# Performance work log

Measured on AMD Instinct MI355X. Metric: run time of the kernel, lower is better.

## Reference

```python
import jax, jax.numpy as jnp
import numpy as np

M, K, N = 4096, 7168, 18432  # tokens, in_features, out_features


def setup_inputs() -> dict:
    key = jax.random.key(0)
    kx, kw, ks = jax.random.split(key, 3)
    x = jax.random.normal(kx, (M, K), dtype=jnp.float32)
    # int8 quantized weight, layout [in_features, out_features] as in the torch module
    weight = jax.random.randint(kw, (K, N), -128, 128, dtype=jnp.int8)
    # per-output-channel dequant scale (bf16 in the original; fp32 here for a stable baseline)
    scale = jax.random.uniform(ks, (N,), dtype=jnp.float32) * 0.02 + 1e-3
    return {"x": x, "weight": weight, "scale": scale}


def reference(x, weight, scale):
    # Fused dequant + GEMM: y = x @ (int8_weight * scale_per_out_channel)
    w = weight.astype(x.dtype) * scale.astype(x.dtype)[None, :]  # [K, N]
    return x @ w  # [M, N]
```

## Files before the change

### kernel.cpp

```cpp
#include <hip/hip_runtime.h>
#include <hip/hip_bf16.h>
#include <cstdint>
#include <cstddef>

#define M_ 4096
#define K_ 7168
#define N_ 18432
#define NT 56

typedef __attribute__((ext_vector_type(4))) int i32x4;
typedef __attribute__((ext_vector_type(16))) int i32x16;

#define AS1 __attribute__((address_space(1)))
#define AS3 __attribute__((address_space(3)))

__device__ __forceinline__ void gld_lds16(void* lds, const void* g) {
  __builtin_amdgcn_global_load_lds((const AS1 void*)g, (AS3 void*)lds, 16, 0, 0);
}

__global__ __launch_bounds__(256) void quant_x_kernel(const float* __restrict__ x,
                                                      signed char* __restrict__ xq,
                                                      float* __restrict__ sx) {
  const int m = blockIdx.x;
  const float4* row4 = (const float4*)(x + (size_t)m * K_);
  float mx = 0.f;
  for (int i = threadIdx.x; i < K_ / 4; i += 256) {
    float4 v = row4[i];
    mx = fmaxf(mx, fmaxf(fmaxf(fabsf(v.x), fabsf(v.y)), fmaxf(fabsf(v.z), fabsf(v.w))));
  }
#pragma unroll
  for (int d = 1; d < 64; d <<= 1) mx = fmaxf(mx, __shfl_xor(mx, d));
  __shared__ float wred[4];
  if ((threadIdx.x & 63) == 0) wred[threadIdx.x >> 6] = mx;
  __syncthreads();
  mx = fmaxf(fmaxf(wred[0], wred[1]), fmaxf(wred[2], wred[3]));
  const float inv = mx > 0.f ? 127.f / mx : 0.f;
  if (threadIdx.x == 0) sx[m] = mx / 127.f;
  char4* q4 = (char4*)(xq + (size_t)m * K_);
  for (int i = threadIdx.x; i < K_ / 4; i += 256) {
    float4 v = row4[i];
    char4 c;
    c.x = (signed char)__float2int_rn(v.x * inv);
    c.y = (signed char)__float2int_rn(v.y * inv);
    c.z = (signed char)__float2int_rn(v.z * inv);
    c.w = (signed char)__float2int_rn(v.w * inv);
    q4[i] = c;
  }
}

__global__ __launch_bounds__(256) void transpose_w_kernel(const int* __restrict__ W,
                                                          signed char* __restrict__ Wt) {
  __shared__ __align__(16) signed char t[64][80];
  const int k0 = blockIdx.x * 64;
  const int n0 = blockIdx.y * 64;
  const int r = threadIdx.x >> 4;
  const int c4 = (threadIdx.x & 15) * 4;
#pragma unroll
  for (int rr = 0; rr < 4; ++rr) {
    const int row = rr * 16 + r;
    int4 v = *(const int4*)(W + (size_t)(k0 + row) * N_ + n0 + c4);
    t[c4 + 0][row] = (signed char)v.x;
    t[c4 + 1][row] = (signed char)v.y;
    t[c4 + 2][row] = (signed char)v.z;
    t[c4 + 3][row] = (signed char)v.w;
  }
  __syncthreads();
  const int nr = threadIdx.x >> 2;
  const int cb = (threadIdx.x & 3) * 16;
  int4 o = *(const int4*)&t[nr][cb];
  *(int4*)(Wt + (size_t)(n0 + nr) * K_ + k0 + cb) = o;
}

__global__ __launch_bounds__(512, 2) void gemm_i8_kernel(const signed char* __restrict__ Aq,
                                                         const signed char* __restrict__ Bt,
                                                         const float* __restrict__ sx,
                                                         const float* __restrict__ scale,
                                                         float* __restrict__ C) {
  __shared__ __align__(16) signed char lds[131072];

  const int bid = blockIdx.x;
  const int xcd = bid & 7;
  const int j = bid >> 3;
  const int m0 = (j & 15) * 256;
  const int n0 = (xcd * 9 + (j >> 4)) * 256;

  const int tid = threadIdx.x;
  const int w = tid >> 6;
  const int lane = tid & 63;
  const int wr = w >> 2;
  const int wc = w & 3;

  const int fr32 = lane & 31;
  const int kh = lane >> 5;
  const int sw = (fr32 >> 2) & 3;
  const int ps0 = ((kh ^ sw) << 4);
  const int ps1 = ps0 ^ 0x20;
  const int rA = (wr * 128 + fr32) * 64;
  const int rB = 65536 + (wc * 64 + fr32) * 64;

  const int ls16 = (((lane & 3) ^ ((lane >> 4) & 3)) << 4);
  const int pr0 = w * 16 + (lane >> 2);
  const unsigned offA0 = (unsigned)(m0 + pr0) * K_ + ls16;
  const unsigned offA1 = (unsigned)(m0 + 128 + pr0) * K_ + ls16;
  const unsigned offB0 = (unsigned)(n0 + pr0) * K_ + ls16;
  const unsigned offB1 = (unsigned)(n0 + 128 + pr0) * K_ + ls16;

#define STAGE_A(T, KS) do {                                                        \
    const int tc_ = (T) < NT ? (T) : NT - 1;                                       \
    signed char* d_ = lds + (((T) & 1) * 32768 + (KS) * 16384 + w * 1024);         \
    gld_lds16(d_, Aq + (size_t)offA0 + tc_ * 128 + (KS) * 64);                     \
    gld_lds16(d_ + 8192, Aq + (size_t)offA1 + tc_ * 128 + (KS) * 64);              \
  } while (0)
#define STAGE_B(T, KS) do {                                                        \
    const int tc_ = (T) < NT ? (T) : NT - 1;                                       \
    signed char* d_ = lds + (65536 + ((T) & 1) * 32768 + (KS) * 16384 + w * 1024); \
    gld_lds16(d_, Bt + (size_t)offB0 + tc_ * 128 + (KS) * 64);                     \
    gld_lds16(d_ + 8192, Bt + (size_t)offB1 + tc_ * 128 + (KS) * 64);              \
  } while (0)
#define LDFR(FA, FB, P, KST) do {                                                  \
    const signed char* base_ = lds + (P) * 32768 + ((KST) >> 1) * 16384            \
                               + (((KST) & 1) ? ps1 : ps0);                        \
    _Pragma("unroll") for (int mt_ = 0; mt_ < 4; ++mt_)                            \
      FA[mt_] = *(const i32x4*)(base_ + rA + mt_ * 2048);                          \
    _Pragma("unroll") for (int nt_ = 0; nt_ < 2; ++nt_)                            \
      FB[nt_] = *(const i32x4*)(base_ + rB + nt_ * 2048);                          \
  } while (0)
#define MFMA8(FA, FB) do {                                                         \
    __builtin_amdgcn_s_setprio(1);                                                 \
    _Pragma("unroll") for (int mt_ = 0; mt_ < 4; ++mt_)                            \
    _Pragma("unroll") for (int nt_ = 0; nt_ < 2; ++nt_)                            \
      acc[mt_][nt_] = __builtin_amdgcn_mfma_i32_32x32x32_i8(                       \
          FA[mt_], FB[nt_], acc[mt_][nt_], 0, 0, 0);                               \
    __builtin_amdgcn_s_setprio(0);                                                 \
  } while (0)
#define BAR do { asm volatile("" ::: "memory");                                    \
                 __builtin_amdgcn_s_barrier();                                     \
                 asm volatile("" ::: "memory"); } while (0)
#define VM0 asm volatile("s_waitcnt vmcnt(0)" ::: "memory")
#define VM8 asm volatile("s_waitcnt vmcnt(8)" ::: "memory")
#define SB __builtin_amdgcn_sched_barrier(0)

#define KTILE(P, TS) do {                                                          \
    MFMA8(fA0, fB0); LDFR(fA0, fB0, P, 2); SB;              \
    MFMA8(fA1, fB1); LDFR(fA1, fB1, P, 3); SB;              \
    MFMA8(fA0, fB0); SB;                                              \
    MFMA8(fA1, fB1);                                                  \
    VM0;            \
    BAR;                 \
    LDFR(fA0, fB0, (P) ^ 1, 0); LDFR(fA1, fB1, (P) ^ 1, 1); SB;                    \
    STAGE_A(TS, 0); STAGE_B(TS, 0); STAGE_A(TS, 1); STAGE_B(TS, 1);                \
  } while (0)

  i32x16 acc[4][2] = {};
  i32x4 fA0[4], fB0[2], fA1[4], fB1[2];

  STAGE_A(0, 0); STAGE_B(0, 0); STAGE_A(0, 1); STAGE_B(0, 1);
  STAGE_A(1, 0); STAGE_B(1, 0); STAGE_A(1, 1); STAGE_B(1, 1);
  VM8;
  BAR;
  LDFR(fA0, fB0, 0, 0); LDFR(fA1, fB1, 0, 1);
  SB;

  for (int it = 0; it < NT / 2; ++it) {
    const int u = 2 * it;
    KTILE(0, u + 2);
    KTILE(1, u + 3);
  }

  const int mb = m0 + wr * 128;
  const int nb = n0 + wc * 64;
  const int col = lane & 31;
  const int rhi = (lane >> 5) * 4;
  const float scl0 = scale[nb + col];
  const float scl1 = scale[nb + 32 + col];
#pragma unroll
  for (int mt = 0; mt < 4; ++mt) {
#pragma unroll
    for (int r = 0; r < 16; ++r) {
      const int row = mb + mt * 32 + (r & 3) + (r >> 2) * 8 + rhi;
      const float s = sx[row];
      float* out = C + (size_t)row * N_ + nb + col;
      out[0]  = (float)acc[mt][0][r] * s * scl0;
      out[32] = (float)acc[mt][1][r] * s * scl1;
    }
  }
#undef STAGE_A
#undef STAGE_B
#undef LDFR
#undef MFMA8
#undef BAR
#undef VM0
#undef VM8
#undef SB
#undef KTILE
}

__global__ __launch_bounds__(256) void fb_gemm_kernel(const float* __restrict__ X,
                                                      const int* __restrict__ W,
                                                      const float* __restrict__ scale,
                                                      float* __restrict__ Y) {
  __shared__ float xs[16][65];
  __shared__ float ws_[16][65];
  const int bn = blockIdx.x * 64;
  const int bm = blockIdx.y * 64;
  const int tx = threadIdx.x & 15;
  const int ty = threadIdx.x >> 4;
  float acc[4][4] = {};
  for (int k0 = 0; k0 < K_; k0 += 16) {
    for (int i = threadIdx.x; i < 64 * 16; i += 256) {
      int r = i >> 4, c = i & 15;
      xs[c][r] = X[(size_t)(bm + r) * K_ + k0 + c];
    }
    for (int i = threadIdx.x; i < 16 * 64; i += 256) {
      int r = i >> 6, c = i & 63;
      ws_[r][c] = (float)W[(size_t)(k0 + r) * N_ + bn + c];
    }
    __syncthreads();
#pragma unroll
    for (int kk = 0; kk < 16; ++kk) {
      float a[4], b[4];
#pragma unroll
      for (int i = 0; i < 4; ++i) a[i] = xs[kk][ty * 4 + i];
#pragma unroll
      for (int j = 0; j < 4; ++j) b[j] = ws_[kk][tx * 4 + j];
#pragma unroll
      for (int i = 0; i < 4; ++i)
#pragma unroll
        for (int j = 0; j < 4; ++j) acc[i][j] += a[i] * b[j];
    }
    __syncthreads();
  }
#pragma unroll
  for (int i = 0; i < 4; ++i)
#pragma unroll
    for (int j = 0; j < 4; ++j)
      Y[(size_t)(bm + ty * 4 + i) * N_ + bn + tx * 4 + j] = acc[i][j] * scale[bn + tx * 4 + j];
}

extern "C" void kernel_launch(void* const* d_in, const int* in_sizes, int n_in,
                              void* d_out, int out_size, void* d_ws, size_t ws_size,
                              hipStream_t stream) {
  const float* x = (const float*)d_in[0];
  const int* w = (const int*)d_in[1];
  const float* scale = (const float*)d_in[2];
  float* y = (float*)d_out;

  const size_t xq_bytes = (size_t)M_ * K_;
  const size_t sx_off = xq_bytes;
  const size_t wt_off = sx_off + (size_t)M_ * 4;
  const size_t need = wt_off + (size_t)N_ * K_;

  if (ws_size >= need) {
    signed char* xq = (signed char*)d_ws;
    float* sx = (float*)((char*)d_ws + sx_off);
    signed char* wt = (signed char*)((char*)d_ws + wt_off);
    hipLaunchKernelGGL(quant_x_kernel, dim3(M_), dim3(256), 0, stream, x, xq, sx);
    hipLaunchKernelGGL(transpose_w_kernel, dim3(K_ / 64, N_ / 64), dim3(256), 0, stream, w, wt);
    hipLaunchKernelGGL(gemm_i8_kernel, dim3((M_ / 256) * (N_ / 256)), dim3(512), 0, stream,
                       xq, wt, sx, scale, y);
  } else {
    hipLaunchKernelGGL(fb_gemm_kernel, dim3(N_ / 64, M_ / 64), dim3(256), 0, stream,
                       x, w, scale, y);
  }
}
```

Baseline: 773.3 us.

## Halve K tile and LDS footprint to fit two GEMM blocks per CU

Shrinks the per-iteration K tile from 128 to 64 bytes, which halves the double-buffered LDS allocation from 128 KiB to 64 KiB. The aim is to let two 512-thread blocks reside on a CU, as the launch bounds request, so one block's MFMA work can hide the other's loads and barriers. The main loop is restructured so each step issues the prefetch for tile t+2 first, then runs two MFMA groups while reading fragments for the next buffer, then waits and synchronises. In exchange there are twice as many iterations and barriers, and each step has less MFMA work to cover its global-load latency. The buffer being refilled is only protected by the previous step's barrier, with no explicit wait for outstanding LDS reads, so there is a possible race.

```diff
diff --git a/kernel.cpp b/kernel.cpp
--- a/kernel.cpp
+++ b/kernel.cpp
@@ -6,7 +6,7 @@
 #define M_ 4096
 #define K_ 7168
 #define N_ 18432
-#define NT 56
+#define NT 112
 
 typedef __attribute__((ext_vector_type(4))) int i32x4;
 typedef __attribute__((ext_vector_type(16))) int i32x16;
@@ -76,7 +76,7 @@
                                                          const float* __restrict__ sx,
                                                          const float* __restrict__ scale,
                                                          float* __restrict__ C) {
-  __shared__ __align__(16) signed char lds[131072];
+  __shared__ __align__(16) signed char lds[65536];
 
   const int bid = blockIdx.x;
   const int xcd = bid & 7;
@@ -96,7 +96,7 @@
   const int ps0 = ((kh ^ sw) << 4);
   const int ps1 = ps0 ^ 0x20;
   const int rA = (wr * 128 + fr32) * 64;
-  const int rB = 65536 + (wc * 64 + fr32) * 64;
+  const int rB = 16384 + (wc * 64 + fr32) * 64;
 
   const int ls16 = (((lane & 3) ^ ((lane >> 4) & 3)) << 4);
   const int pr0 = w * 16 + (lane >> 2);
@@ -105,21 +105,17 @@
   const unsigned offB0 = (unsigned)(n0 + pr0) * K_ + ls16;
   const unsigned offB1 = (unsigned)(n0 + 128 + pr0) * K_ + ls16;
 
-#define STAGE_A(T, KS) do {                                                        \
+#define STAGE(T, P) do {                                                           \
     const int tc_ = (T) < NT ? (T) : NT - 1;                                       \
-    signed char* d_ = lds + (((T) & 1) * 32768 + (KS) * 16384 + w * 1024);         \
-    gld_lds16(d_, Aq + (size_t)offA0 + tc_ * 128 + (KS) * 64);                     \
-    gld_lds16(d_ + 8192, Aq + (size_t)offA1 + tc_ * 128 + (KS) * 64);              \
-  } while (0)
-#define STAGE_B(T, KS) do {                                                        \
-    const int tc_ = (T) < NT ? (T) : NT - 1;                                       \
-    signed char* d_ = lds + (65536 + ((T) & 1) * 32768 + (KS) * 16384 + w * 1024); \
-    gld_lds16(d_, Bt + (size_t)offB0 + tc_ * 128 + (KS) * 64);                     \
-    gld_lds16(d_ + 8192, Bt + (size_t)offB1 + tc_ * 128 + (KS) * 64);              \
+    signed char* dA_ = lds + (P) * 32768 + w * 1024;                               \
+    gld_lds16(dA_, Aq + (size_t)offA0 + tc_ * 64);                                 \
+    gld_lds16(dA_ + 8192, Aq + (size_t)offA1 + tc_ * 64);                          \
+    signed char* dB_ = dA_ + 16384;                                                \
+    gld_lds16(dB_, Bt + (size_t)offB0 + tc_ * 64);                                 \
+    gld_lds16(dB_ + 8192, Bt + (size_t)offB1 + tc_ * 64);                          \
   } while (0)
 #define LDFR(FA, FB, P, KST) do {                                                  \
-    const signed char* base_ = lds + (P) * 32768 + ((KST) >> 1) * 16384            \
-                               + (((KST) & 1) ? ps1 : ps0);                        \
+    const signed char* base_ = lds + (P) * 32768 + ((KST) ? ps1 : ps0);            \
     _Pragma("unroll") for (int mt_ = 0; mt_ < 4; ++mt_)                            \
       FA[mt_] = *(const i32x4*)(base_ + rA + mt_ * 2048);                          \
     _Pragma("unroll") for (int nt_ = 0; nt_ < 2; ++nt_)                            \
@@ -137,34 +133,30 @@
                  __builtin_amdgcn_s_barrier();                                     \
                  asm volatile("" ::: "memory"); } while (0)
 #define VM0 asm volatile("s_waitcnt vmcnt(0)" ::: "memory")
-#define VM8 asm volatile("s_waitcnt vmcnt(8)" ::: "memory")
+#define LGKM0 asm volatile("s_waitcnt lgkmcnt(0)" ::: "memory")
 #define SB __builtin_amdgcn_sched_barrier(0)
 
-#define KTILE(P, TS) do {                                                          \
-    MFMA8(fA0, fB0); LDFR(fA0, fB0, P, 2); SB;              \
-    MFMA8(fA1, fB1); LDFR(fA1, fB1, P, 3); SB;              \
-    MFMA8(fA0, fB0); SB;                                              \
-    MFMA8(fA1, fB1);                                                  \
-    VM0;            \
-    BAR;                 \
-    LDFR(fA0, fB0, (P) ^ 1, 0); LDFR(fA1, fB1, (P) ^ 1, 1); SB;                    \
-    STAGE_A(TS, 0); STAGE_B(TS, 0); STAGE_A(TS, 1); STAGE_B(TS, 1);                \
+#define KTILE(P, T) do {                                                           \
+    STAGE((T) + 2, P); SB;                                                         \
+    MFMA8(fA0, fB0); LDFR(fA0, fB0, (P) ^ 1, 0); SB;                               \
+    MFMA8(fA1, fB1); LDFR(fA1, fB1, (P) ^ 1, 1); SB;                               \
+    VM0;                        \
+    BAR;                      \
   } while (0)
 
   i32x16 acc[4][2] = {};
   i32x4 fA0[4], fB0[2], fA1[4], fB1[2];
 
-  STAGE_A(0, 0); STAGE_B(0, 0); STAGE_A(0, 1); STAGE_B(0, 1);
-  STAGE_A(1, 0); STAGE_B(1, 0); STAGE_A(1, 1); STAGE_B(1, 1);
-  VM8;
+  STAGE(0, 0); STAGE(1, 1);
+  VM0;
   BAR;
   LDFR(fA0, fB0, 0, 0); LDFR(fA1, fB1, 0, 1);
-  SB;
-
-  for (int it = 0; it < NT / 2; ++it) {
-    const int u = 2 * it;
-    KTILE(0, u + 2);
-    KTILE(1, u + 3);
+  LGKM0; SB;
+  BAR;
+
+  for (int t = 0; t < NT; t += 2) {
+    KTILE(0, t);
+    KTILE(1, t + 1);
   }
 
   const int mb = m0 + wr * 128;
@@ -184,13 +176,12 @@
       out[32] = (float)acc[mt][1][r] * s * scl1;
     }
   }
-#undef STAGE_A
-#undef STAGE_B
+#undef STAGE
 #undef LDFR
 #undef MFMA8
 #undef BAR
 #undef VM0
-#undef VM8
+#undef LGKM0
 #undef SB
 #undef KTILE
 }
```

Measured after the change: 787.3 us. No clear change (+1.8%).
